# Optimization experiments

Hardware: AMD Instinct MI355X
Metric: run time of the kernel (lower is better)

Reference implementation:

```python
import math
import jax, jax.numpy as jnp
import numpy as np


def _conv2d_same(x, w):
    # x: [B,C,H,W], w: [O,I,3,3] -> [B,O,H,W], stride 1, padding 1 (SAME)
    return jax.lax.conv_general_dilated(
        x, w, window_strides=(1, 1), padding='SAME',
        dimension_numbers=('NCHW', 'OIHW', 'NCHW'))


def setup_inputs() -> dict:
    key = jax.random.key(0)
    ks = jax.random.split(key, 7)
    B, CK, CV, T, H, W = 2, 64, 512, 8, 48, 48
    mk = jax.random.normal(ks[0], (B, CK, T, H, W), dtype=jnp.float32)
    qk = jax.random.normal(ks[1], (B, CK, H, W), dtype=jnp.float32)
    mv = jax.random.normal(ks[2], (B, CV, T, H, W), dtype=jnp.float32)
    qv = jax.random.normal(ks[3], (B, CV, H, W), dtype=jnp.float32)
    mask = jax.random.uniform(ks[4], (B, 1, H, W), dtype=jnp.float32)
    conv_w = jax.random.normal(ks[5], (1, 2 * CV + 1, 3, 3), dtype=jnp.float32) * 0.02
    conv_b = jnp.zeros((1,), dtype=jnp.float32)
    return {"mk": mk, "qk": qk, "mv": mv, "qv": qv, "mask": mask,
            "conv_w": conv_w, "conv_b": conv_b}


def reference(mk, qk, mv, qv, mask, conv_w, conv_b):
    B, CK, T, H, W = mk.shape
    CV = mv.shape[1]
    M, N = T * H * W, H * W  # memory tokens, query tokens

    # --- MemoryReader.get_affinity: L2-expanded attention over memory axis ---
    mkf = mk.reshape(B, CK, M)           # [B,CK,M]
    qkf = qk.reshape(B, CK, N)           # [B,CK,N]
    a_sq = jnp.sum(mkf * mkf, axis=1)[:, :, None]            # [B,M,1]
    ab = jnp.einsum('bcm,bcn->bmn', mkf, qkf)                # [B,M,N]
    affinity = (2.0 * ab - a_sq) / math.sqrt(CK)
    affinity = jax.nn.softmax(affinity, axis=1)              # softmax over memory tokens

    # --- MemoryReader.readout: bmm readout + concat with query value ---
    mo = mv.reshape(B, CV, M)                                # [B,CV,M]
    mem = jnp.einsum('bcm,bmn->bcn', mo, affinity).reshape(B, CV, H, W)
    mem_out = jnp.concatenate([mem, qv], axis=1)             # [B,2*CV,H,W]

    # --- STCN.segment gating chain: conv(cat(mem, mask)) -> sigmoid -> gate ---
    gate_in = jnp.concatenate([mem_out, mask], axis=1)       # [B,2*CV+1,H,W]
    gate = jax.nn.sigmoid(_conv2d_same(gate_in, conv_w) + conv_b[None, :, None, None])
    return mem_out * gate
```

## Files before the change

kernel.cpp:

```cpp
#include <hip/hip_runtime.h>

#define B_  2
#define CK_ 64
#define CV_ 512
#define H_  48
#define W_  48
#define M_  18432
#define N_  2304

#define VSTRIDE16 (CV_ * 16)

typedef __bf16 bf16x8 __attribute__((ext_vector_type(8)));
typedef float  f32x4  __attribute__((ext_vector_type(4)));
typedef float  f32x16 __attribute__((ext_vector_type(16)));
typedef unsigned int u32x4 __attribute__((ext_vector_type(4)));

#define C2Q   0.36067376f
#define C_KSQ 0.18033688f

__device__ inline f32x16 mfma32(bf16x8 a, bf16x8 b, f32x16 c) {
    return __builtin_amdgcn_mfma_f32_32x32x16_bf16(a, b, c, 0, 0, 0);
}

__device__ inline unsigned pack_bf16(float lo, float hi) {
    union { __bf16 h; unsigned short u; } a, b;
    a.h = (__bf16)lo; b.h = (__bf16)hi;
    return ((unsigned)b.u << 16) | a.u;
}

__device__ __forceinline__ void gload_lds16(const __bf16* g, __bf16* l) {
    __builtin_amdgcn_global_load_lds(
        (const __attribute__((address_space(1))) void*)g,
        (__attribute__((address_space(3))) void*)l,
        16, 0, 0);
}

__global__ __launch_bounds__(256) void prep_k(const float* __restrict__ mk,
                                              __bf16* __restrict__ ktile,
                                              unsigned* __restrict__ ksq2) {
    const int idx = blockIdx.x * 256 + threadIdx.x;
    const int b = idx / M_, m = idx % M_;
    const float* src = mk + (size_t)b * CK_ * M_ + m;
    const int mt = m >> 5, l = m & 31;
    __bf16* dstb = ktile + (size_t)b * M_ * 64 + (size_t)mt * 2048 + l * 8;
    float s = 0.f;
#pragma unroll
    for (int j = 0; j < 8; ++j) {
        bf16x8 o;
#pragma unroll
        for (int i = 0; i < 8; ++i) {
            float v = src[(size_t)(8 * j + i) * M_];
            s += v * v;
            o[i] = (__bf16)v;
        }
        *(bf16x8*)(dstb + (size_t)j * 256) = o;
    }
    const float tot = s * C_KSQ;
    const float hi = (float)(__bf16)tot;
    const float lo = tot - hi;
    ksq2[idx] = pack_bf16(hi, lo);
}

__global__ __launch_bounds__(256) void prep_v(const float* __restrict__ mv,
                                              __bf16* __restrict__ vt) {
    const int idx = blockIdx.x * 256 + threadIdx.x;
    const int c   = idx % CV_;
    const int r   = idx / CV_;
    const int m16 = r % (M_ / 16);
    const int b   = r / (M_ / 16);
    const float4* s4 = (const float4*)(mv + ((size_t)b * CV_ + c) * M_ + m16 * 16);
    const float4 a0 = s4[0], a1 = s4[1], a2 = s4[2], a3 = s4[3];
    bf16x8 o0, o1;
    o0[0]=(__bf16)a0.x; o0[1]=(__bf16)a0.y; o0[2]=(__bf16)a0.z; o0[3]=(__bf16)a0.w;
    o0[4]=(__bf16)a1.x; o0[5]=(__bf16)a1.y; o0[6]=(__bf16)a1.z; o0[7]=(__bf16)a1.w;
    o1[0]=(__bf16)a2.x; o1[1]=(__bf16)a2.y; o1[2]=(__bf16)a2.z; o1[3]=(__bf16)a2.w;
    o1[4]=(__bf16)a3.x; o1[5]=(__bf16)a3.y; o1[6]=(__bf16)a3.z; o1[7]=(__bf16)a3.w;
    __bf16* dst = vt + ((size_t)r * CV_ + c) * 16;
    *(bf16x8*)dst = o0;
    *(bf16x8*)(dst + 8) = o1;
}


#define LOADK() do {                                                          \
    kC0 = *(const bf16x8*)(kp + koff);                                        \
    kC1 = *(const bf16x8*)(kp + koff + 512);                                  \
    kC2 = *(const bf16x8*)(kp + koff + 1024);                                 \
    kC3 = *(const bf16x8*)(kp + koff + 1536);                                 \
    kqC = kqp[l31];                                                           \
    kp += 2048; kqp += 32;                                                    \
} while (0)

#define STAGEV(vnxt) do {                                                     \
    _Pragma("unroll")                                                         \
    for (int i = 0; i < 4; ++i) {                                             \
        const int jj = i * 4 + w;                                             \
        const int chunk = jj >> 3, off = jj & 7;                              \
        gload_lds16(vps + chunk * VSTRIDE16 + cwoff + off * 512 + soff,       \
                    (vnxt) + chunk * 4096 + off * 512);                       \
    }                                                                         \
    vps += 2 * VSTRIDE16;                                                     \
} while (0)

__global__ __launch_bounds__(256, 2) void flash15_kernel(const __bf16* __restrict__ ktile,
                                                         const float* __restrict__ qk,
                                                         const __bf16* __restrict__ vt,
                                                         const unsigned* __restrict__ ksq2,
                                                         __bf16* __restrict__ partO,
                                                         float* __restrict__ partD) {
    const int tid = threadIdx.x;
    const int w = tid >> 6, lane = tid & 63;
    const int l31 = lane & 31, h = lane >> 5;

    const int bid = blockIdx.x;
    const int x = bid & 7;
    const int j = bid >> 3;
    int col, slot;
    if (j < 8) { col = x;                slot = x * 8 + j; }
    else {
        const int c_loc = (j - 8) / 7, idx7 = (j - 8) % 7;
        col = 8 + x * 8 + c_loc;
        slot = 64 + (col - 8) * 7 + idx7;
    }
    const int base = (col < 8) ? col * 8 : 64 + (col - 8) * 7;
    const int idx  = slot - base;
    const int cnt  = (col < 8) ? 8 : 7;
    const int ntg  = col % 18;
    const int cb   = col / 18;
    const int cs2  = cb & 1, b = cb >> 1;
    const int nt   = ntg * 4 + w;

    int s0, ns;
    if (cnt == 8) { s0 = idx * 72; ns = 72; }
    else if (idx < 2) { s0 = idx * 83; ns = 83; }
    else { s0 = 166 + (idx - 2) * 82; ns = 82; }

    const int n0 = nt * 32;
    const int cw = cs2 * 256;

    const int koff  = (h * 32 + l31) * 8;
    const int vloff = lane * 8;
    const int cwoff = cw * 16;
    const int soff  = (lane & 31) * 16 + (lane >> 5) * 8;

    __shared__ __align__(16) __bf16 Vlds[2][8192];

    const float* qkb = qk + (size_t)b * CK_ * N_;
    bf16x8 qf[4];
#pragma unroll
    for (int ks = 0; ks < 4; ++ks)
#pragma unroll
      for (int i = 0; i < 8; ++i)
        qf[ks][i] = (__bf16)(qkb[(size_t)(16*ks + 8*h + i) * N_ + (n0 + l31)] * C2Q);

    const u32x4 bneg_u = {0xBF80BF80u, 0u, 0u, 0u};
    const bf16x8 bneg = __builtin_bit_cast(bf16x8, bneg_u);

    const __bf16*   kp  = ktile + (size_t)b * M_ * 64 + (size_t)s0 * 2048;
    const unsigned* kqp = ksq2  + (size_t)b * M_ + s0 * 32;
    const __bf16*   vps = vt    + (size_t)b * M_ * CV_ + (size_t)s0 * 2 * VSTRIDE16;

    f32x16 acc[8];
#pragma unroll
    for (int ct = 0; ct < 8; ++ct)
#pragma unroll
      for (int r = 0; r < 16; ++r) acc[ct][r] = 0.f;
    float den[4] = {0.f, 0.f, 0.f, 0.f};

    bf16x8 kC0, kC1, kC2, kC3;
    unsigned kqC;
    bf16x8 va[4], vb[4];

    LOADK();
    STAGEV(&Vlds[0][0]);
    const __bf16* vc = &Vlds[0][0];
    __bf16* vn = &Vlds[1][0];

    for (int s = 0; s < ns; ++s) {
        __syncthreads();
        const int more = (s + 1 < ns);
        if (more) STAGEV(vn);
        u32x4 a4u = { h ? 0u : kqC, 0u, 0u, 0u };
        const bf16x8 af4 = __builtin_bit_cast(bf16x8, a4u);
        f32x16 d;
#pragma unroll
        for (int r = 0; r < 16; ++r) d[r] = 0.f;
        __builtin_amdgcn_s_setprio(1);
        d = mfma32(af4, bneg, d);
        d = mfma32(kC0, qf[0], d);
        d = mfma32(kC1, qf[1], d);
        d = mfma32(kC2, qf[2], d);
        d = mfma32(kC3, qf[3], d);
        __builtin_amdgcn_s_setprio(0);
        if (more) LOADK();
        unsigned wpk[8];
#pragma unroll
        for (int jj = 0; jj < 8; ++jj) {
            const float pa = __builtin_amdgcn_exp2f(d[2*jj]);
            const float pc = __builtin_amdgcn_exp2f(d[2*jj+1]);
            den[jj & 3] += pa + pc;
            wpk[jj] = pack_bf16(pa, pc);
        }
        bf16x8 pb0, pb1;
        {
            unsigned a0 = wpk[0], b0 = wpk[2];
            unsigned a1 = wpk[1], b1 = wpk[3];
            asm volatile("v_permlane32_swap_b32 %0, %1" : "+v"(a0), "+v"(b0));
            asm volatile("v_permlane32_swap_b32 %0, %1" : "+v"(a1), "+v"(b1));
            u32x4 pu = {a0, a1, b0, b1};
            pb0 = __builtin_bit_cast(bf16x8, pu);
        }
        {
            unsigned a0 = wpk[4], b0 = wpk[6];
            unsigned a1 = wpk[5], b1 = wpk[7];
            asm volatile("v_permlane32_swap_b32 %0, %1" : "+v"(a0), "+v"(b0));
            asm volatile("v_permlane32_swap_b32 %0, %1" : "+v"(a1), "+v"(b1));
            u32x4 pu = {a0, a1, b0, b1};
            pb1 = __builtin_bit_cast(bf16x8, pu);
        }
#pragma unroll
        for (int jj = 0; jj < 4; ++jj)
            va[jj] = *(const bf16x8*)(vc + jj * 512 + vloff);
#pragma unroll
        for (int jj = 0; jj < 4; ++jj)
            vb[jj] = *(const bf16x8*)(vc + (4 + jj) * 512 + vloff);
        __builtin_amdgcn_s_setprio(1);
#pragma unroll
        for (int jj = 0; jj < 4; ++jj)
            acc[jj] = mfma32(va[jj], pb0, acc[jj]);
        __builtin_amdgcn_s_setprio(0);
#pragma unroll
        for (int jj = 0; jj < 4; ++jj)
            va[jj] = *(const bf16x8*)(vc + 4096 + jj * 512 + vloff);
        __builtin_amdgcn_s_setprio(1);
#pragma unroll
        for (int jj = 0; jj < 4; ++jj)
            acc[4 + jj] = mfma32(vb[jj], pb0, acc[4 + jj]);
        __builtin_amdgcn_s_setprio(0);
#pragma unroll
        for (int jj = 0; jj < 4; ++jj)
            vb[jj] = *(const bf16x8*)(vc + 4096 + (4 + jj) * 512 + vloff);
        __builtin_amdgcn_s_setprio(1);
#pragma unroll
        for (int jj = 0; jj < 4; ++jj)
            acc[jj] = mfma32(va[jj], pb1, acc[jj]);
#pragma unroll
        for (int jj = 0; jj < 4; ++jj)
            acc[4 + jj] = mfma32(vb[jj], pb1, acc[4 + jj]);
        __builtin_amdgcn_s_setprio(0);
        __bf16* t = (__bf16*)vc; vc = vn; vn = t;
    }

    float dsum = (den[0] + den[1]) + (den[2] + den[3]);
    dsum += __shfl_xor(dsum, 32);
    if (cs2 == 0 && lane < 32)
        partD[(size_t)slot * 128 + w * 32 + l31] = dsum;

    __bf16* po = partO + (size_t)slot * 32768 + (w * 32 + l31);
#pragma unroll
    for (int ct = 0; ct < 8; ++ct)
#pragma unroll
      for (int r = 0; r < 16; ++r) {
        const int ch = 32*ct + (r & 3) + 8*(r >> 2) + 4*h;
        po[(size_t)ch * 128] = (__bf16)acc[ct][r];
      }
}

__global__ __launch_bounds__(256) void reduce_kernel(const __bf16* __restrict__ partO,
                                                     const float* __restrict__ partD,
                                                     float* __restrict__ out) {
    const int idx = blockIdx.x * 256 + threadIdx.x;
    const int n8 = idx % (N_ / 8);
    const int c  = (idx / (N_ / 8)) % CV_;
    const int b  = idx / ((N_ / 8) * CV_);
    const int n  = n8 * 8;
    const int ntg = n / 128, nl = n % 128;
    const int cs2 = c >> 8, chloc = c & 255;

    const int col  = ntg + 18 * (cs2 + 2 * b);
    const int colD = ntg + 36 * b;
    const int baseO = (col  < 8) ? col  * 8 : 64 + (col  - 8) * 7;
    const int cntO  = (col  < 8) ? 8 : 7;
    const int baseD = (colD < 8) ? colD * 8 : 64 + (colD - 8) * 7;
    const int cntD  = (colD < 8) ? 8 : 7;

    float o[8] = {0,0,0,0,0,0,0,0};
    for (int i = 0; i < cntO; ++i) {
        const bf16x8 ov = *(const bf16x8*)(partO + (size_t)(baseO + i) * 32768
                                           + chloc * 128 + nl);
#pragma unroll
        for (int jj = 0; jj < 8; ++jj) o[jj] += (float)ov[jj];
    }
    float dd[8] = {0,0,0,0,0,0,0,0};
    for (int i = 0; i < cntD; ++i) {
        const float4 d0 = *(const float4*)(partD + (size_t)(baseD + i) * 128 + nl);
        const float4 d1 = *(const float4*)(partD + (size_t)(baseD + i) * 128 + nl + 4);
        dd[0]+=d0.x; dd[1]+=d0.y; dd[2]+=d0.z; dd[3]+=d0.w;
        dd[4]+=d1.x; dd[5]+=d1.y; dd[6]+=d1.z; dd[7]+=d1.w;
    }
    float* op = out + ((size_t)b * (2*CV_) + c) * N_ + n;
#pragma unroll
    for (int jj = 0; jj < 8; ++jj) op[jj] = o[jj] / dd[jj];
}

__global__ __launch_bounds__(256) void conv_r_kernel(const float* __restrict__ outf,
                                                     const float* __restrict__ qv,
                                                     const float* __restrict__ mask,
                                                     const float* __restrict__ cw,
                                                     float* __restrict__ Rp) {
    const int p  = blockIdx.x * 256 + threadIdx.x;
    const int cc = blockIdx.y;
    const int b  = blockIdx.z;
    float r[9] = {0,0,0,0,0,0,0,0,0};
    if (cc < 8) {
        const float* src = (cc < 4) ? outf + ((size_t)b * (2*CV_) + cc * 128) * N_
                                    : qv   + ((size_t)b * CV_ + (cc - 4) * 128) * N_;
        const float* wb = cw + (size_t)cc * 128 * 9;
        for (int c = 0; c < 128; ++c) {
            const float v = src[(size_t)c * N_ + p];
#pragma unroll
            for (int jj = 0; jj < 9; ++jj) r[jj] += v * wb[c * 9 + jj];
        }
    } else {
        const float v = mask[(size_t)b * N_ + p];
#pragma unroll
        for (int jj = 0; jj < 9; ++jj) r[jj] = v * cw[1024 * 9 + jj];
    }
#pragma unroll
    for (int jj = 0; jj < 9; ++jj)
        Rp[(((size_t)cc * 9 + jj) * B_ + b) * N_ + p] = r[jj];
}

__global__ __launch_bounds__(256) void gate_kernel(const float* __restrict__ Rp,
                                                   const float* __restrict__ cbias,
                                                   float* __restrict__ gate_ws) {
    const int p = blockIdx.x * 256 + threadIdx.x;
    const int b = blockIdx.y;
    const int y = p / W_, x = p % W_;
    float sum = cbias[0];
#pragma unroll
    for (int dy = -1; dy <= 1; ++dy) {
        const int yy = y + dy;
        if (yy < 0 || yy >= H_) continue;
#pragma unroll
        for (int dx = -1; dx <= 1; ++dx) {
            const int xx = x + dx;
            if (xx < 0 || xx >= W_) continue;
            const int jj = (dy + 1) * 3 + (dx + 1);
            const int q = yy * W_ + xx;
#pragma unroll
            for (int cc = 0; cc < 9; ++cc)
                sum += Rp[(((size_t)cc * 9 + jj) * B_ + b) * N_ + q];
        }
    }
    gate_ws[(size_t)b * N_ + p] = 1.f / (1.f + __builtin_amdgcn_exp2f(-sum * 1.44269504f));
}

__global__ __launch_bounds__(256) void finalize_kernel(const float* __restrict__ qv,
                                                       const float* __restrict__ gate_ws,
                                                       float* __restrict__ out) {
    const int idx = blockIdx.x * 256 + threadIdx.x;
    const int n4 = N_ / 4;
    const int pos4 = idx % n4;
    const int row  = idx / n4;
    const int b = row >> 10, ch = row & 1023;
    const float4 gv = *(const float4*)(gate_ws + (size_t)b * N_ + pos4 * 4);
    float* op = out + (size_t)row * N_ + pos4 * 4;
    float4 v;
    if (ch < CV_) v = *(const float4*)op;
    else          v = *(const float4*)(qv + ((size_t)b * CV_ + (ch - CV_)) * N_ + pos4 * 4);
    v.x *= gv.x; v.y *= gv.y; v.z *= gv.z; v.w *= gv.w;
    *(float4*)op = v;
}

extern "C" void kernel_launch(void* const* d_in, const int* in_sizes, int n_in,
                              void* d_out, int out_size, void* d_ws, size_t ws_size,
                              hipStream_t stream) {
    (void)in_sizes; (void)n_in; (void)out_size; (void)ws_size;
    const float* mk    = (const float*)d_in[0];
    const float* qk    = (const float*)d_in[1];
    const float* mv    = (const float*)d_in[2];
    const float* qv    = (const float*)d_in[3];
    const float* mask  = (const float*)d_in[4];
    const float* cw    = (const float*)d_in[5];
    const float* cbias = (const float*)d_in[6];
    float* outf = (float*)d_out;

    const size_t kbf_b   = (size_t)B_ * M_ * 64 * 2;
    const size_t vbf_b   = (size_t)B_ * CV_ * M_ * 2;
    const size_t ksq_b   = (size_t)B_ * M_ * 4;
    const size_t partO_b = (size_t)512 * 32768 * 2;
    const size_t partD_b = (size_t)512 * 128 * 4;

    char* pw = (char*)d_ws;
    __bf16* ktile = (__bf16*)pw;
    float*  Rp    = (float*)pw;
    pw += kbf_b;
    __bf16* vt    = (__bf16*)pw;           pw += vbf_b;
    unsigned* ksq2 = (unsigned*)pw;        pw += ksq_b;
    __bf16* partO = (__bf16*)pw;           pw += partO_b;
    float*  partD = (float*)pw;            pw += partD_b;
    float*  gate_ws = (float*)pw;

    prep_k<<<dim3(B_ * M_ / 256), 256, 0, stream>>>(mk, ktile, ksq2);
    prep_v<<<dim3((size_t)B_ * (M_ / 16) * CV_ / 256, 1, 1), 256, 0, stream>>>(mv, vt);
    flash15_kernel<<<dim3(512), 256, 0, stream>>>(ktile, qk, vt, ksq2, partO, partD);
    reduce_kernel<<<dim3(B_ * CV_ * (N_ / 8) / 256), 256, 0, stream>>>(partO, partD, outf);
    conv_r_kernel<<<dim3(N_ / 256, 9, B_), 256, 0, stream>>>(outf, qv, mask, cw, Rp);
    gate_kernel<<<dim3(N_ / 256, B_), 256, 0, stream>>>(Rp, cbias, gate_ws);
    finalize_kernel<<<dim3((B_ * 2 * CV_ * N_ / 4) / 256), 256, 0, stream>>>(qv, gate_ws, outf);
}
```

Measured before the change: 198.3 us.

## Software-pipeline flash loop across iterations and merge K/V prep kernels

Restructures the main attention loop so that the QK score MFMA and exp/pack for step s overlap with the PV MFMAs for step s-1. This needs a triple-buffered V tile in LDS (three 16 KB buffers instead of two) plus a prologue and epilogue. It also fuses the separate K and V bf16 conversion kernels into one launch split by block index. The aim is to hide exp/transcendental latency behind matrix work and save a launch. The cost is more LDS per block, which may hurt the two-blocks-per-CU occupancy, and more live registers.

Measured after the change: 197.6 us. No clear change (-0.3%).

```diff
diff --git a/kernel.cpp b/kernel.cpp
--- a/kernel.cpp
+++ b/kernel.cpp
@@ -9,6 +9,7 @@
 #define N_  2304
 
 #define VSTRIDE16 (CV_ * 16)
+#define KPBLKS    (B_ * M_ / 256)
 
 typedef __bf16 bf16x8 __attribute__((ext_vector_type(8)));
 typedef float  f32x4  __attribute__((ext_vector_type(4)));
@@ -35,49 +36,50 @@
         16, 0, 0);
 }
 
-__global__ __launch_bounds__(256) void prep_k(const float* __restrict__ mk,
-                                              __bf16* __restrict__ ktile,
-                                              unsigned* __restrict__ ksq2) {
-    const int idx = blockIdx.x * 256 + threadIdx.x;
-    const int b = idx / M_, m = idx % M_;
-    const float* src = mk + (size_t)b * CK_ * M_ + m;
-    const int mt = m >> 5, l = m & 31;
-    __bf16* dstb = ktile + (size_t)b * M_ * 64 + (size_t)mt * 2048 + l * 8;
-    float s = 0.f;
-#pragma unroll
-    for (int j = 0; j < 8; ++j) {
-        bf16x8 o;
-#pragma unroll
-        for (int i = 0; i < 8; ++i) {
-            float v = src[(size_t)(8 * j + i) * M_];
-            s += v * v;
-            o[i] = (__bf16)v;
+__global__ __launch_bounds__(256) void prep_kv(const float* __restrict__ mk,
+                                               const float* __restrict__ mv,
+                                               __bf16* __restrict__ ktile,
+                                               unsigned* __restrict__ ksq2,
+                                               __bf16* __restrict__ vt) {
+    if (blockIdx.x < KPBLKS) {
+        const int idx = blockIdx.x * 256 + threadIdx.x;
+        const int b = idx / M_, m = idx % M_;
+        const float* src = mk + (size_t)b * CK_ * M_ + m;
+        const int mt = m >> 5, l = m & 31;
+        __bf16* dstb = ktile + (size_t)b * M_ * 64 + (size_t)mt * 2048 + l * 8;
+        float s = 0.f;
+#pragma unroll
+        for (int j = 0; j < 8; ++j) {
+            bf16x8 o;
+#pragma unroll
+            for (int i = 0; i < 8; ++i) {
+                float v = src[(size_t)(8 * j + i) * M_];
+                s += v * v;
+                o[i] = (__bf16)v;
+            }
+            *(bf16x8*)(dstb + (size_t)j * 256) = o;
         }
-        *(bf16x8*)(dstb + (size_t)j * 256) = o;
-    }
-    const float tot = s * C_KSQ;
-    const float hi = (float)(__bf16)tot;
-    const float lo = tot - hi;
-    ksq2[idx] = pack_bf16(hi, lo);
-}
-
-__global__ __launch_bounds__(256) void prep_v(const float* __restrict__ mv,
-                                              __bf16* __restrict__ vt) {
-    const int idx = blockIdx.x * 256 + threadIdx.x;
-    const int c   = idx % CV_;
-    const int r   = idx / CV_;
-    const int m16 = r % (M_ / 16);
-    const int b   = r / (M_ / 16);
-    const float4* s4 = (const float4*)(mv + ((size_t)b * CV_ + c) * M_ + m16 * 16);
-    const float4 a0 = s4[0], a1 = s4[1], a2 = s4[2], a3 = s4[3];
-    bf16x8 o0, o1;
-    o0[0]=(__bf16)a0.x; o0[1]=(__bf16)a0.y; o0[2]=(__bf16)a0.z; o0[3]=(__bf16)a0.w;
-    o0[4]=(__bf16)a1.x; o0[5]=(__bf16)a1.y; o0[6]=(__bf16)a1.z; o0[7]=(__bf16)a1.w;
-    o1[0]=(__bf16)a2.x; o1[1]=(__bf16)a2.y; o1[2]=(__bf16)a2.z; o1[3]=(__bf16)a2.w;
-    o1[4]=(__bf16)a3.x; o1[5]=(__bf16)a3.y; o1[6]=(__bf16)a3.z; o1[7]=(__bf16)a3.w;
-    __bf16* dst = vt + ((size_t)r * CV_ + c) * 16;
-    *(bf16x8*)dst = o0;
-    *(bf16x8*)(dst + 8) = o1;
+        const float tot = s * C_KSQ;
+        const float hi = (float)(__bf16)tot;
+        const float lo = tot - hi;
+        ksq2[idx] = pack_bf16(hi, lo);
+    } else {
+        const int idx = (blockIdx.x - KPBLKS) * 256 + threadIdx.x;
+        const int c   = idx % CV_;
+        const int r   = idx / CV_;
+        const int m16 = r % (M_ / 16);
+        const int b   = r / (M_ / 16);
+        const float4* s4 = (const float4*)(mv + ((size_t)b * CV_ + c) * M_ + m16 * 16);
+        const float4 a0 = s4[0], a1 = s4[1], a2 = s4[2], a3 = s4[3];
+        bf16x8 o0, o1;
+        o0[0]=(__bf16)a0.x; o0[1]=(__bf16)a0.y; o0[2]=(__bf16)a0.z; o0[3]=(__bf16)a0.w;
+        o0[4]=(__bf16)a1.x; o0[5]=(__bf16)a1.y; o0[6]=(__bf16)a1.z; o0[7]=(__bf16)a1.w;
+        o1[0]=(__bf16)a2.x; o1[1]=(__bf16)a2.y; o1[2]=(__bf16)a2.z; o1[3]=(__bf16)a2.w;
+        o1[4]=(__bf16)a3.x; o1[5]=(__bf16)a3.y; o1[6]=(__bf16)a3.z; o1[7]=(__bf16)a3.w;
+        __bf16* dst = vt + ((size_t)r * CV_ + c) * 16;
+        *(bf16x8*)dst = o0;
+        *(bf16x8*)(dst + 8) = o1;
+    }
 }
 
 
@@ -101,7 +103,63 @@
     vps += 2 * VSTRIDE16;                                                     \
 } while (0)
 
-__global__ __launch_bounds__(256, 2) void flash15_kernel(const __bf16* __restrict__ ktile,
+#define QKC() do {                                                            \
+    u32x4 a4u = { h ? 0u : kqC, 0u, 0u, 0u };                                 \
+    const bf16x8 af4 = __builtin_bit_cast(bf16x8, a4u);                       \
+    _Pragma("unroll") for (int r = 0; r < 16; ++r) d[r] = 0.f;                \
+    __builtin_amdgcn_s_setprio(1);                                            \
+    d = mfma32(af4, bneg, d);                                                 \
+    d = mfma32(kC0, qf[0], d);                                                \
+    d = mfma32(kC1, qf[1], d);                                                \
+    d = mfma32(kC2, qf[2], d);                                                \
+    d = mfma32(kC3, qf[3], d);                                                \
+    __builtin_amdgcn_s_setprio(0);                                            \
+} while (0)
+
+#define EXPPACK(P0, P1) do {                                                  \
+    unsigned wpk[8];                                                          \
+    _Pragma("unroll")                                                         \
+    for (int jj = 0; jj < 8; ++jj) {                                          \
+        const float pa = __builtin_amdgcn_exp2f(d[2*jj]);                     \
+        const float pc = __builtin_amdgcn_exp2f(d[2*jj+1]);                   \
+        den[jj & 3] += pa + pc;                                               \
+        wpk[jj] = pack_bf16(pa, pc);                                          \
+    }                                                                         \
+    {                                                                         \
+        unsigned a0 = wpk[0], b0 = wpk[2], a1 = wpk[1], b1 = wpk[3];          \
+        asm volatile("v_permlane32_swap_b32 %0, %1" : "+v"(a0), "+v"(b0));    \
+        asm volatile("v_permlane32_swap_b32 %0, %1" : "+v"(a1), "+v"(b1));    \
+        u32x4 pu = {a0, a1, b0, b1};                                          \
+        P0 = __builtin_bit_cast(bf16x8, pu);                                  \
+    }                                                                         \
+    {                                                                         \
+        unsigned a0 = wpk[4], b0 = wpk[6], a1 = wpk[5], b1 = wpk[7];          \
+        asm volatile("v_permlane32_swap_b32 %0, %1" : "+v"(a0), "+v"(b0));    \
+        asm volatile("v_permlane32_swap_b32 %0, %1" : "+v"(a1), "+v"(b1));    \
+        u32x4 pu = {a0, a1, b0, b1};                                          \
+        P1 = __builtin_bit_cast(bf16x8, pu);                                  \
+    }                                                                         \
+} while (0)
+
+#define PVQ(vbase, off, P, a0i) do {                                          \
+    _Pragma("unroll")                                                         \
+    for (int jj = 0; jj < 4; ++jj)                                            \
+        va[jj] = *(const bf16x8*)((vbase) + (off) + jj * 512 + vloff);        \
+    __builtin_amdgcn_s_setprio(1);                                            \
+    _Pragma("unroll")                                                         \
+    for (int jj = 0; jj < 4; ++jj)                                            \
+        acc[(a0i) + jj] = mfma32(va[jj], P, acc[(a0i) + jj]);                 \
+    __builtin_amdgcn_s_setprio(0);                                            \
+} while (0)
+
+#define PVBLOCK(vbase) do {                                                   \
+    PVQ((vbase), 0,    pbP0, 0);                                              \
+    PVQ((vbase), 2048, pbP0, 4);                                              \
+    PVQ((vbase), 4096, pbP1, 0);                                              \
+    PVQ((vbase), 6144, pbP1, 4);                                              \
+} while (0)
+
+__global__ __launch_bounds__(256, 2) void flash16_kernel(const __bf16* __restrict__ ktile,
                                                          const float* __restrict__ qk,
                                                          const __bf16* __restrict__ vt,
                                                          const unsigned* __restrict__ ksq2,
@@ -142,7 +200,7 @@
     const int cwoff = cw * 16;
     const int soff  = (lane & 31) * 16 + (lane >> 5) * 8;
 
-    __shared__ __align__(16) __bf16 Vlds[2][8192];
+    __shared__ __align__(16) __bf16 Vlds[3][8192];
 
     const float* qkb = qk + (size_t)b * CK_ * N_;
     bf16x8 qf[4];
@@ -168,87 +226,34 @@
 
     bf16x8 kC0, kC1, kC2, kC3;
     unsigned kqC;
-    bf16x8 va[4], vb[4];
+    bf16x8 va[4];
+    f32x16 d;
+    bf16x8 pbP0, pbP1;
 
     LOADK();
     STAGEV(&Vlds[0][0]);
-    const __bf16* vc = &Vlds[0][0];
-    __bf16* vn = &Vlds[1][0];
-
-    for (int s = 0; s < ns; ++s) {
+    STAGEV(&Vlds[1][0]);
+    QKC();
+    LOADK();
+    EXPPACK(pbP0, pbP1);
+
+    const __bf16* vm1  = &Vlds[0][0];
+    const __bf16* vcur = &Vlds[1][0];
+    __bf16*       vnxt = &Vlds[2][0];
+
+    for (int s = 1; s < ns; ++s) {
         __syncthreads();
         const int more = (s + 1 < ns);
-        if (more) STAGEV(vn);
-        u32x4 a4u = { h ? 0u : kqC, 0u, 0u, 0u };
-        const bf16x8 af4 = __builtin_bit_cast(bf16x8, a4u);
-        f32x16 d;
-#pragma unroll
-        for (int r = 0; r < 16; ++r) d[r] = 0.f;
-        __builtin_amdgcn_s_setprio(1);
-        d = mfma32(af4, bneg, d);
-        d = mfma32(kC0, qf[0], d);
-        d = mfma32(kC1, qf[1], d);
-        d = mfma32(kC2, qf[2], d);
-        d = mfma32(kC3, qf[3], d);
-        __builtin_amdgcn_s_setprio(0);
+        if (more) STAGEV(vnxt);
+        QKC();
         if (more) LOADK();
-        unsigned wpk[8];
-#pragma unroll
-        for (int jj = 0; jj < 8; ++jj) {
-            const float pa = __builtin_amdgcn_exp2f(d[2*jj]);
-            const float pc = __builtin_amdgcn_exp2f(d[2*jj+1]);
-            den[jj & 3] += pa + pc;
-            wpk[jj] = pack_bf16(pa, pc);
-        }
-        bf16x8 pb0, pb1;
-        {
-            unsigned a0 = wpk[0], b0 = wpk[2];
-            unsigned a1 = wpk[1], b1 = wpk[3];
-            asm volatile("v_permlane32_swap_b32 %0, %1" : "+v"(a0), "+v"(b0));
-            asm volatile("v_permlane32_swap_b32 %0, %1" : "+v"(a1), "+v"(b1));
-            u32x4 pu = {a0, a1, b0, b1};
-            pb0 = __builtin_bit_cast(bf16x8, pu);
-        }
-        {
-            unsigned a0 = wpk[4], b0 = wpk[6];
-            unsigned a1 = wpk[5], b1 = wpk[7];
-            asm volatile("v_permlane32_swap_b32 %0, %1" : "+v"(a0), "+v"(b0));
-            asm volatile("v_permlane32_swap_b32 %0, %1" : "+v"(a1), "+v"(b1));
-            u32x4 pu = {a0, a1, b0, b1};
-            pb1 = __builtin_bit_cast(bf16x8, pu);
-        }
-#pragma unroll
-        for (int jj = 0; jj < 4; ++jj)
-            va[jj] = *(const bf16x8*)(vc + jj * 512 + vloff);
-#pragma unroll
-        for (int jj = 0; jj < 4; ++jj)
-            vb[jj] = *(const bf16x8*)(vc + (4 + jj) * 512 + vloff);
-        __builtin_amdgcn_s_setprio(1);
-#pragma unroll
-        for (int jj = 0; jj < 4; ++jj)
-            acc[jj] = mfma32(va[jj], pb0, acc[jj]);
-        __builtin_amdgcn_s_setprio(0);
-#pragma unroll
-        for (int jj = 0; jj < 4; ++jj)
-            va[jj] = *(const bf16x8*)(vc + 4096 + jj * 512 + vloff);
-        __builtin_amdgcn_s_setprio(1);
-#pragma unroll
-        for (int jj = 0; jj < 4; ++jj)
-            acc[4 + jj] = mfma32(vb[jj], pb0, acc[4 + jj]);
-        __builtin_amdgcn_s_setprio(0);
-#pragma unroll
-        for (int jj = 0; jj < 4; ++jj)
-            vb[jj] = *(const bf16x8*)(vc + 4096 + (4 + jj) * 512 + vloff);
-        __builtin_amdgcn_s_setprio(1);
-#pragma unroll
-        for (int jj = 0; jj < 4; ++jj)
-            acc[jj] = mfma32(va[jj], pb1, acc[jj]);
-#pragma unroll
-        for (int jj = 0; jj < 4; ++jj)
-            acc[4 + jj] = mfma32(vb[jj], pb1, acc[4 + jj]);
-        __builtin_amdgcn_s_setprio(0);
-        __bf16* t = (__bf16*)vc; vc = vn; vn = t;
-    }
+        PVBLOCK(vm1);
+        bf16x8 pbC0, pbC1;
+        EXPPACK(pbC0, pbC1);
+        pbP0 = pbC0; pbP1 = pbC1;
+        __bf16* t = (__bf16*)vm1; vm1 = vcur; vcur = vnxt; vnxt = t;
+    }
+    PVBLOCK(vm1);
 
     float dsum = (den[0] + den[1]) + (den[2] + den[3]);
     dsum += __shfl_xor(dsum, 32);
@@ -401,9 +406,9 @@
     float*  partD = (float*)pw;            pw += partD_b;
     float*  gate_ws = (float*)pw;
 
-    prep_k<<<dim3(B_ * M_ / 256), 256, 0, stream>>>(mk, ktile, ksq2);
-    prep_v<<<dim3((size_t)B_ * (M_ / 16) * CV_ / 256, 1, 1), 256, 0, stream>>>(mv, vt);
-    flash15_kernel<<<dim3(512), 256, 0, stream>>>(ktile, qk, vt, ksq2, partO, partD);
+    const int vblocks = (int)((size_t)B_ * (M_ / 16) * CV_ / 256);
+    prep_kv<<<dim3(KPBLKS + vblocks), 256, 0, stream>>>(mk, mv, ktile, ksq2, vt);
+    flash16_kernel<<<dim3(512), 256, 0, stream>>>(ktile, qk, vt, ksq2, partO, partD);
     reduce_kernel<<<dim3(B_ * CV_ * (N_ / 8) / 256), 256, 0, stream>>>(partO, partD, outf);
     conv_r_kernel<<<dim3(N_ / 256, 9, B_), 256, 0, stream>>>(outf, qv, mask, cw, Rp);
     gate_kernel<<<dim3(N_ / 256, B_), 256, 0, stream>>>(Rp, cbias, gate_ws);
```
